# Kernel tuning notes

Measured on AMD Instinct MI355X. Metric: run time of the kernel, lower is better.

Reference implementation:

```python
import jax, jax.numpy as jnp
import numpy as np

B, N, D = 32, 4096, 256
HEADS, DH = 4, 64
DI = HEADS * DH  # 256
SLOTS, ITERS, EPS, HID = 8, 3, 1e-8, 128


def _ln(x, w, b):
    m = jnp.mean(x, axis=-1, keepdims=True)
    v = jnp.mean(jnp.square(x - m), axis=-1, keepdims=True)
    return (x - m) * jax.lax.rsqrt(v + 1e-5) * w + b


def setup_inputs() -> dict:
    key = jax.random.key(0)
    ks = jax.random.split(key, 12)
    g = lambda k, shape, s=0.05: jax.random.normal(k, shape, jnp.float32) * s
    return {
        "inputs": jax.random.normal(ks[0], (B, N, D), jnp.float32),
        "slots_mu": jax.random.normal(ks[1], (1, 1, D), jnp.float32),
        "slots_logsigma": g(ks[2], (1, 1, D), 0.1),
        "ln_in_w": jnp.ones((D,)), "ln_in_b": jnp.zeros((D,)),
        "ln_s_w": jnp.ones((D,)), "ln_s_b": jnp.zeros((D,)),
        "Wq": g(ks[3], (D, DI)), "Wk": g(ks[4], (D, DI)), "Wv": g(ks[5], (D, DI)),
        "Wc": g(ks[6], (DI, D)),
        "gru_w_ih": g(ks[7], (3 * D, D)), "gru_w_hh": g(ks[8], (3 * D, D)),
        "gru_b_ih": jnp.zeros((3 * D,)), "gru_b_hh": jnp.zeros((3 * D,)),
        "ln_m_w": jnp.ones((D,)), "ln_m_b": jnp.zeros((D,)),
        "mlp_w1": g(ks[9], (D, HID)), "mlp_b1": jnp.zeros((HID,)),
        "mlp_w2": g(ks[10], (HID, D)), "mlp_b2": jnp.zeros((D,)),
    }


def reference(inputs, slots_mu, slots_logsigma, ln_in_w, ln_in_b, ln_s_w, ln_s_b,
              Wq, Wk, Wv, Wc, gru_w_ih, gru_w_hh, gru_b_ih, gru_b_hh,
              ln_m_w, ln_m_b, mlp_w1, mlp_b1, mlp_w2, mlp_b2):
    b, n, d = inputs.shape
    scale = DH ** -0.5
    # slot initialization (fixed-seed gaussian, mirrors torch.manual_seed(0))
    noise = jax.random.normal(jax.random.key(42), (b, SLOTS, d), inputs.dtype)
    slots = slots_mu + jnp.exp(slots_logsigma) * noise

    x = _ln(inputs, ln_in_w, ln_in_b)
    k = (x @ Wk).reshape(b, n, HEADS, DH).transpose(0, 2, 1, 3)  # b h n dh
    v = (x @ Wv).reshape(b, n, HEADS, DH).transpose(0, 2, 1, 3)  # b h n dh

    for _ in range(ITERS):
        slots_prev = slots
        s = _ln(slots, ln_s_w, ln_s_b)
        q = (s @ Wq).reshape(b, SLOTS, HEADS, DH).transpose(0, 2, 1, 3)  # b h s dh
        dots = jnp.einsum('bhid,bhjd->bhij', q, k) * scale  # b h slots n
        attn = jax.nn.softmax(dots, axis=-2)  # softmax over SLOTS axis
        attn = attn + EPS
        attn = attn / jnp.sum(attn, axis=-1, keepdims=True)  # L1 norm over tokens
        updates = jnp.einsum('bhjd,bhij->bhid', v, attn)  # b h slots dh
        updates = updates.transpose(0, 2, 1, 3).reshape(b, SLOTS, DI) @ Wc  # b s d

        # GRUCell (PyTorch gate ordering: r, z, n)
        u = updates.reshape(-1, d)
        h = slots_prev.reshape(-1, d)
        gx = u @ gru_w_ih.T + gru_b_ih
        gh = h @ gru_w_hh.T + gru_b_hh
        xr, xz, xn = jnp.split(gx, 3, axis=-1)
        hr, hz, hn = jnp.split(gh, 3, axis=-1)
        r = jax.nn.sigmoid(xr + hr)
        z = jax.nn.sigmoid(xz + hz)
        ng = jnp.tanh(xn + r * hn)
        slots = ((1.0 - z) * ng + z * h).reshape(b, SLOTS, d)

        m = _ln(slots, ln_m_w, ln_m_b)
        slots = slots + (jax.nn.relu(m @ mlp_w1 + mlp_b1) @ mlp_w2 + mlp_b2)
    return slots
```

## Files before the change

kernel.cpp:

```cpp
#include <hip/hip_runtime.h>
#include <hip/hip_bf16.h>
#include <stdint.h>

constexpr int B_ = 32, N_ = 4096, D_ = 256, NH_ = 4, DH_ = 64, NS_ = 8;
constexpr float EPS_ = 1e-8f;

typedef unsigned short u16;
typedef __attribute__((ext_vector_type(8))) short bf16x8;
typedef __attribute__((ext_vector_type(4))) float f32x4;

__device__ inline u16 f2bf(float f) {
  unsigned u = __float_as_uint(f);
  unsigned r = u + 0x7FFFu + ((u >> 16) & 1u);
  return (u16)(r >> 16);
}
__device__ inline float bf2f(u16 u) {
  return __uint_as_float(((unsigned)u) << 16);
}

__device__ inline float erfinv_f(float x) {
  float w = -logf((1.0f - x) * (1.0f + x));
  float p;
  if (w < 5.0f) {
    w = w - 2.5f;
    p = 2.81022636e-08f;
    p = 3.43273939e-07f + p * w;
    p = -3.5233877e-06f + p * w;
    p = -4.39150654e-06f + p * w;
    p = 0.00021858087f + p * w;
    p = -0.00125372503f + p * w;
    p = -0.00417768164f + p * w;
    p = 0.246640727f + p * w;
    p = 1.50140941f + p * w;
  } else {
    w = sqrtf(w) - 3.0f;
    p = -0.000200214257f;
    p = 0.000100950558f + p * w;
    p = 0.00134934322f + p * w;
    p = -0.00367342844f + p * w;
    p = 0.00573950773f + p * w;
    p = -0.0076224613f + p * w;
    p = 0.00943887047f + p * w;
    p = 1.00167406f + p * w;
    p = 2.83297682f + p * w;
  }
  return p * x;
}

__device__ inline void threefry(unsigned k0, unsigned k1, unsigned& x0, unsigned& x1) {
  unsigned ks2 = k0 ^ k1 ^ 0x1BD11BDAu;
  x0 += k0; x1 += k1;
#define TF_R(r) { x0 += x1; x1 = (x1 << (r)) | (x1 >> (32 - (r))); x1 ^= x0; }
  TF_R(13) TF_R(15) TF_R(26) TF_R(6)
  x0 += k1; x1 += ks2 + 1u;
  TF_R(17) TF_R(29) TF_R(16) TF_R(24)
  x0 += ks2; x1 += k0 + 2u;
  TF_R(13) TF_R(15) TF_R(26) TF_R(6)
  x0 += k0; x1 += k1 + 3u;
  TF_R(17) TF_R(29) TF_R(16) TF_R(24)
  x0 += k1; x1 += ks2 + 4u;
  TF_R(13) TF_R(15) TF_R(26) TF_R(6)
  x0 += ks2; x1 += k0 + 5u;
#undef TF_R
}

__device__ inline float bits_to_normal(unsigned bits) {
  float f = __uint_as_float((bits >> 9) | 0x3F800000u) - 1.0f;
  const float lo = -0.99999994f;
  const float span = 2.0f;
  float u = fmaxf(lo, f * span + lo);
  return 1.41421356f * erfinv_f(u);
}

__global__ __launch_bounds__(256) void k_slots_init(const float* __restrict__ mu,
                                                    const float* __restrict__ logsigma,
                                                    float* __restrict__ slots) {
  unsigned e = blockIdx.x * 256u + threadIdx.x;
  unsigned x0 = 0u, x1 = e;
  threefry(0u, 42u, x0, x1);
  unsigned bits = x0 ^ x1;
  float n = bits_to_normal(bits);
  int d = e & 255;
  slots[e] = mu[d] + expf(logsigma[d]) * n;
}

__global__ __launch_bounds__(256) void k_qproj(const float* __restrict__ slots,
                                               const float* __restrict__ ln_w,
                                               const float* __restrict__ ln_b,
                                               const float* __restrict__ Wq,
                                               float* __restrict__ qout) {
  __shared__ float sn[256];
  __shared__ float redA[4], redB[4];
  int row = blockIdx.x, t = threadIdx.x;
  float x = slots[row * 256 + t];
  float s = x, s2 = x * x;
#pragma unroll
  for (int off = 32; off; off >>= 1) { s += __shfl_xor(s, off); s2 += __shfl_xor(s2, off); }
  if ((t & 63) == 0) { redA[t >> 6] = s; redB[t >> 6] = s2; }
  __syncthreads();
  float ts = redA[0] + redA[1] + redA[2] + redA[3];
  float ts2 = redB[0] + redB[1] + redB[2] + redB[3];
  float m = ts * (1.0f / 256.0f);
  float var = ts2 * (1.0f / 256.0f) - m * m;
  float rstd = rsqrtf(var + 1e-5f);
  sn[t] = (x - m) * rstd * ln_w[t] + ln_b[t];
  __syncthreads();
  float a = 0.0f;
  for (int k = 0; k < 256; ++k) a += sn[k] * Wq[k * 256 + t];
  qout[row * 256 + t] = a * 0.125f;
}

__global__ __launch_bounds__(256) void k_qproj2(const float* __restrict__ slots,
                                                const float* __restrict__ ln_w,
                                                const float* __restrict__ ln_b,
                                                const float* __restrict__ Wq,
                                                float* __restrict__ qout) {
  __shared__ float sn[256];
  __shared__ float part[4][64];
  __shared__ float redA[4], redB[4];
  int row = blockIdx.x, g = blockIdx.y, t = threadIdx.x;
  float x = slots[row * 256 + t];
  float s = x, s2 = x * x;
#pragma unroll
  for (int off = 32; off; off >>= 1) { s += __shfl_xor(s, off); s2 += __shfl_xor(s2, off); }
  if ((t & 63) == 0) { redA[t >> 6] = s; redB[t >> 6] = s2; }
  __syncthreads();
  float ts = redA[0] + redA[1] + redA[2] + redA[3];
  float ts2 = redB[0] + redB[1] + redB[2] + redB[3];
  float m = ts * (1.0f / 256.0f);
  float var = ts2 * (1.0f / 256.0f) - m * m;
  float rstd = rsqrtf(var + 1e-5f);
  sn[t] = (x - m) * rstd * ln_w[t] + ln_b[t];
  __syncthreads();
  int c = t & 63, kq = t >> 6;
  int col = g * 64 + c;
  float a = 0.0f;
#pragma unroll 8
  for (int k = kq * 64; k < kq * 64 + 64; ++k) a += sn[k] * Wq[k * 256 + col];
  part[kq][c] = a;
  __syncthreads();
  if (t < 64)
    qout[row * 256 + g * 64 + t] =
        (part[0][t] + part[1][t] + part[2][t] + part[3][t]) * 0.125f;
}

__global__ __launch_bounds__(256) void k_wt(const float* __restrict__ Wk,
                                            const float* __restrict__ Wv,
                                            u16* __restrict__ Wt) {
  int n = blockIdx.x;
  int t = threadIdx.x;
  const float* src = blockIdx.y ? Wv : Wk;
  Wt[((blockIdx.y * 256 + n) << 8) + t] = f2bf(src[t * 256 + n]);
}

__global__ __launch_bounds__(64) void k_wt2(const float* __restrict__ Wk,
                                            const float* __restrict__ Wv,
                                            u16* __restrict__ Wt2) {
  int cb = blockIdx.x, m = blockIdx.y, ks = blockIdx.z;
  int lane = threadIdx.x;
  const float* W = m ? Wv : Wk;
  int col = cb * 16 + (lane & 15);
  int kbase = ks * 32 + (lane >> 4) * 8;
  unsigned pk[4];
#pragma unroll
  for (int j = 0; j < 4; ++j) {
    u16 lo = f2bf(W[(long)(kbase + 2 * j) * 256 + col]);
    u16 hi = f2bf(W[(long)(kbase + 2 * j + 1) * 256 + col]);
    pk[j] = (unsigned)lo | ((unsigned)hi << 16);
  }
  *(uint4*)&Wt2[(long)(((m * 16 + cb) * 8 + ks) * 64 + lane) * 8] =
      make_uint4(pk[0], pk[1], pk[2], pk[3]);
}

__global__ __launch_bounds__(256) void k_gru_t(const float* __restrict__ src,
                                               float* __restrict__ dst) {
  __shared__ float tile[32][33];
  int c0 = blockIdx.x * 32;
  int r0 = blockIdx.y * 32;
  int tx = threadIdx.x & 31, ty = threadIdx.x >> 5;
#pragma unroll
  for (int i = 0; i < 32; i += 8)
    tile[ty + i][tx] = src[(long)(r0 + ty + i) * 256 + c0 + tx];
  __syncthreads();
#pragma unroll
  for (int i = 0; i < 32; i += 8)
    dst[(long)(c0 + ty + i) * 768 + r0 + tx] = tile[tx][ty + i];
}

__global__ __launch_bounds__(512, 4) void k_proj_mfma3(
    const float* __restrict__ in,
    const float* __restrict__ ln_w, const float* __restrict__ ln_b,
    const u16* __restrict__ Wt2,
    u16* __restrict__ kbuf, u16* __restrict__ vbuf) {
  constexpr int LDA = 264;
  __shared__ __align__(16) u16 lds[18432];
  u16* Asm = lds;
  int t = threadIdx.x;
  int w = t >> 6, lane = t & 63;
  int q = lane >> 4, r = lane & 15;
  long row0 = (long)blockIdx.x * 64;
  int m = w >> 2;

  float4 lw = ((const float4*)ln_w)[lane];
  float4 lb = ((const float4*)ln_b)[lane];
  float4 vr[8];
#pragma unroll
  for (int j = 0; j < 8; ++j)
    vr[j] = ((const float4*)(in + (row0 + w * 8 + j) * D_))[lane];
#pragma unroll
  for (int j = 0; j < 8; ++j) {
    int rr = w * 8 + j;
    float4 v = vr[j];
    float s = v.x + v.y + v.z + v.w;
    float s2 = v.x * v.x + v.y * v.y + v.z * v.z + v.w * v.w;
#pragma unroll
    for (int off = 32; off; off >>= 1) { s += __shfl_xor(s, off); s2 += __shfl_xor(s2, off); }
    float mn = s * (1.0f / 256.0f);
    float var = s2 * (1.0f / 256.0f) - mn * mn;
    float rstd = rsqrtf(var + 1e-5f);
    unsigned p0 = (unsigned)f2bf((v.x - mn) * rstd * lw.x + lb.x)
                | ((unsigned)f2bf((v.y - mn) * rstd * lw.y + lb.y) << 16);
    unsigned p1 = (unsigned)f2bf((v.z - mn) * rstd * lw.z + lb.z)
                | ((unsigned)f2bf((v.w - mn) * rstd * lw.w + lb.w) << 16);
    *(uint2*)&Asm[rr * LDA + lane * 4] = make_uint2(p0, p1);
  }
  __syncthreads();

  f32x4 acc[4][4];
#pragma unroll
  for (int mf = 0; mf < 4; ++mf)
#pragma unroll
    for (int nf = 0; nf < 4; ++nf) acc[mf][nf] = (f32x4)0.0f;

#pragma unroll 2
  for (int ks = 0; ks < 8; ++ks) {
    int k0 = ks * 32;
    bf16x8 a[4], b[4];
#pragma unroll
    for (int mf = 0; mf < 4; ++mf)
      a[mf] = *(const bf16x8*)&Asm[(mf * 16 + r) * LDA + k0 + q * 8];
#pragma unroll
    for (int nf = 0; nf < 4; ++nf)
      b[nf] = *(const bf16x8*)&Wt2[(long)(((m * 16 + (w & 3) * 4 + nf) * 8 + ks) * 64 + lane) * 8];
#pragma unroll
    for (int mf = 0; mf < 4; ++mf)
#pragma unroll
      for (int nf = 0; nf < 4; ++nf)
        acc[mf][nf] = __builtin_amdgcn_mfma_f32_16x16x32_bf16(a[mf], b[nf], acc[mf][nf], 0, 0, 0);
  }

  __syncthreads();
  u16* st = lds + w * 2304;
  u16* outp = m ? vbuf : kbuf;
  int colbase = (w & 3) * 64;
#pragma unroll
  for (int p = 0; p < 2; ++p) {
#pragma unroll
    for (int mfh = 0; mfh < 2; ++mfh) {
      int mf = p * 2 + mfh;
#pragma unroll
      for (int nf = 0; nf < 4; ++nf)
#pragma unroll
        for (int rr = 0; rr < 4; ++rr) {
          int rowp = mfh * 16 + q * 4 + rr;
          int col = nf * 16 + r;
          int colsw = col ^ ((rowp & 7) << 3);
          st[rowp * 72 + colsw] = f2bf(acc[mf][nf][rr]);
        }
    }
#pragma unroll
    for (int sub = 0; sub < 4; ++sub) {
      int rowp = sub * 8 + (lane >> 3);
      int c8 = (lane & 7) * 8;
      int c8s = c8 ^ ((rowp & 7) << 3);
      uint4 val = *(const uint4*)&st[rowp * 72 + c8s];
      *(uint4*)&outp[(row0 + p * 32 + rowp) * 256 + colbase + c8] = val;
    }
  }
}

__global__ __launch_bounds__(512, 4) void k_proj_mfma2(
    const float* __restrict__ in,
    const float* __restrict__ ln_w, const float* __restrict__ ln_b,
    const u16* __restrict__ Wt,
    u16* __restrict__ kbuf, u16* __restrict__ vbuf) {
  constexpr int LDA = 264;
  __shared__ __align__(16) u16 Asm[64 * LDA];
  int t = threadIdx.x;
  int w = t >> 6, lane = t & 63;
  int q = lane >> 4, r = lane & 15;
  long row0 = (long)blockIdx.x * 64;
  int half = blockIdx.y;

  float4 lw = ((const float4*)ln_w)[lane];
  float4 lb = ((const float4*)ln_b)[lane];
#pragma unroll 4
  for (int j = 0; j < 8; ++j) {
    int rr = w * 8 + j;
    float4 v = ((const float4*)(in + (row0 + rr) * D_))[lane];
    float s = v.x + v.y + v.z + v.w;
    float s2 = v.x * v.x + v.y * v.y + v.z * v.z + v.w * v.w;
#pragma unroll
    for (int off = 32; off; off >>= 1) { s += __shfl_xor(s, off); s2 += __shfl_xor(s2, off); }
    float m = s * (1.0f / 256.0f);
    float var = s2 * (1.0f / 256.0f) - m * m;
    float rstd = rsqrtf(var + 1e-5f);
    unsigned p0 = (unsigned)f2bf((v.x - m) * rstd * lw.x + lb.x)
                | ((unsigned)f2bf((v.y - m) * rstd * lw.y + lb.y) << 16);
    unsigned p1 = (unsigned)f2bf((v.z - m) * rstd * lw.z + lb.z)
                | ((unsigned)f2bf((v.w - m) * rstd * lw.w + lb.w) << 16);
    *(uint2*)&Asm[rr * LDA + lane * 4] = make_uint2(p0, p1);
  }
  __syncthreads();

  f32x4 acc[4][2];
#pragma unroll
  for (int mf = 0; mf < 4; ++mf)
#pragma unroll
    for (int nf = 0; nf < 2; ++nf) acc[mf][nf] = (f32x4)0.0f;

  const u16* wt_base = Wt + (long)(half * 256 + w * 32) * 256;
#pragma unroll 2
  for (int k0 = 0; k0 < 256; k0 += 32) {
    bf16x8 a[4], b[2];
#pragma unroll
    for (int mf = 0; mf < 4; ++mf)
      a[mf] = *(const bf16x8*)&Asm[(mf * 16 + r) * LDA + k0 + q * 8];
#pragma unroll
    for (int nf = 0; nf < 2; ++nf)
      b[nf] = *(const bf16x8*)&wt_base[(nf * 16 + r) * 256 + k0 + q * 8];
#pragma unroll
    for (int mf = 0; mf < 4; ++mf)
#pragma unroll
      for (int nf = 0; nf < 2; ++nf)
        acc[mf][nf] = __builtin_amdgcn_mfma_f32_16x16x32_bf16(a[mf], b[nf], acc[mf][nf], 0, 0, 0);
  }

  __syncthreads();
  u16* st = Asm + w * 1280;
  u16* outp = half ? vbuf : kbuf;
#pragma unroll
  for (int p = 0; p < 2; ++p) {
#pragma unroll
    for (int m2 = 0; m2 < 2; ++m2)
#pragma unroll
      for (int nf = 0; nf < 2; ++nf)
#pragma unroll
        for (int rr = 0; rr < 4; ++rr)
          st[(m2 * 16 + q * 4 + rr) * 40 + nf * 16 + r] = f2bf(acc[p * 2 + m2][nf][rr]);
#pragma unroll
    for (int s = 0; s < 2; ++s) {
      int rw = s * 16 + (lane >> 2);
      int cc = (lane & 3) * 8;
      uint4 val = *(const uint4*)&st[rw * 40 + cc];
      *(uint4*)&outp[(row0 + p * 32 + rw) * 256 + w * 32 + cc] = val;
    }
  }
}

__global__ __launch_bounds__(256) void k_attn(
    const float* __restrict__ qbuf,
    const u16* __restrict__ kbuf, const u16* __restrict__ vbuf,
    float* __restrict__ U, float* __restrict__ S) {
  __shared__ float redS[2048];
  __shared__ float sredS[32];
  int b = blockIdx.y, chunk = blockIdx.x;
  int t = threadIdx.x;
  int wave = t >> 6, lane = t & 63;

  for (int e = t; e < 2048; e += 256) redS[e] = 0.0f;
  if (t < 32) sredS[t] = 0.0f;

  float qv[8][4];
#pragma unroll
  for (int i = 0; i < 8; ++i) {
    float4 qq = *(const float4*)(qbuf + ((long)(b * 8 + i)) * 256 + lane * 4);
    qv[i][0] = qq.x; qv[i][1] = qq.y; qv[i][2] = qq.z; qv[i][3] = qq.w;
  }
  float acc[8][4];
  float sacc[8];
#pragma unroll
  for (int i = 0; i < 8; ++i) {
    sacc[i] = 0.0f;
    acc[i][0] = acc[i][1] = acc[i][2] = acc[i][3] = 0.0f;
  }
  __syncthreads();

  long jbase = (long)b * N_ + chunk * 128;
  for (int jj = wave; jj < 128; jj += 4) {
    long off = (jbase + jj) * 256 + lane * 4;
    ushort4 k4 = *(const ushort4*)(kbuf + off);
    ushort4 v4 = *(const ushort4*)(vbuf + off);
    float k0 = bf2f(k4.x), k1 = bf2f(k4.y), k2 = bf2f(k4.z), k3 = bf2f(k4.w);

    float d[8];
#pragma unroll
    for (int i = 0; i < 8; ++i)
      d[i] = qv[i][0] * k0 + qv[i][1] * k1 + qv[i][2] * k2 + qv[i][3] * k3;
#pragma unroll
    for (int off2 = 1; off2 < 16; off2 <<= 1) {
#pragma unroll
      for (int i = 0; i < 8; ++i) d[i] += __shfl_xor(d[i], off2);
    }
    float mx = d[0];
#pragma unroll
    for (int i = 1; i < 8; ++i) mx = fmaxf(mx, d[i]);
    float e[8], sum = 0.0f;
#pragma unroll
    for (int i = 0; i < 8; ++i) { e[i] = expf(d[i] - mx); sum += e[i]; }
    float inv = 1.0f / sum;

    float v0 = bf2f(v4.x), v1 = bf2f(v4.y), v2 = bf2f(v4.z), v3 = bf2f(v4.w);
#pragma unroll
    for (int i = 0; i < 8; ++i) {
      float a = e[i] * inv + EPS_;
      sacc[i] += a;
      acc[i][0] += a * v0; acc[i][1] += a * v1; acc[i][2] += a * v2; acc[i][3] += a * v3;
    }
  }

#pragma unroll
  for (int i = 0; i < 8; ++i) {
    atomicAdd(&redS[i * 256 + lane * 4 + 0], acc[i][0]);
    atomicAdd(&redS[i * 256 + lane * 4 + 1], acc[i][1]);
    atomicAdd(&redS[i * 256 + lane * 4 + 2], acc[i][2]);
    atomicAdd(&redS[i * 256 + lane * 4 + 3], acc[i][3]);
  }
  if ((lane & 15) == 0) {
    int h = lane >> 4;
#pragma unroll
    for (int i = 0; i < 8; ++i) atomicAdd(&sredS[i * 4 + h], sacc[i]);
  }
  __syncthreads();

  for (int e = t; e < 2048; e += 256)
    atomicAdd(&U[((long)b * 8 + (e >> 8)) * 256 + (e & 255)], redS[e]);
  if (t < 32) atomicAdd(&S[b * 32 + t], sredS[t]);
}

__global__ __launch_bounds__(256) void k_attn3(
    const float* __restrict__ qbuf,
    const u16* __restrict__ kbuf, const u16* __restrict__ vbuf,
    float* __restrict__ P, float* __restrict__ Sp) {
  __shared__ __align__(16) u16 Ks[64 * 260];
  __shared__ __align__(16) float qs[8 * 256];
  __shared__ float dw[64 * 33];
  int b = blockIdx.y, chunk = blockIdx.x;
  int t = threadIdx.x;
  int tok = t & 63;
  int sp = t >> 6;

  for (int e = t; e < 2048; e += 256) qs[e] = qbuf[(long)b * 2048 + e];

  float acc0[4] = {0.f, 0.f, 0.f, 0.f};
  float acc1[4] = {0.f, 0.f, 0.f, 0.f};
  float rden[8] = {0.f, 0.f, 0.f, 0.f, 0.f, 0.f, 0.f, 0.f};

  long tokbase = (long)b * N_ + chunk * 128;
  for (int tile = 0; tile < 2; ++tile) {
    long trow = tokbase + tile * 64;
    __syncthreads();
#pragma unroll
    for (int i = 0; i < 16; ++i) {
      int idx = i * 256 + t;
      int row = idx >> 6, c8 = idx & 63;
      *(uint2*)&Ks[row * 260 + c8 * 4] =
          *(const uint2*)&kbuf[(trow + row) * 256 + c8 * 4];
    }
    __syncthreads();

    float d0[4] = {0.f, 0.f, 0.f, 0.f};
    float d1[4] = {0.f, 0.f, 0.f, 0.f};
#pragma unroll
    for (int h = 0; h < 4; ++h) {
#pragma unroll
      for (int c2 = 0; c2 < 8; ++c2) {
        int cc = h * 8 + c2;
        ushort4 ka = *(const ushort4*)&Ks[tok * 260 + cc * 8];
        ushort4 kb = *(const ushort4*)&Ks[tok * 260 + cc * 8 + 4];
        float k0 = bf2f(ka.x), k1 = bf2f(ka.y), k2 = bf2f(ka.z), k3 = bf2f(ka.w);
        float k4 = bf2f(kb.x), k5 = bf2f(kb.y), k6 = bf2f(kb.z), k7 = bf2f(kb.w);
        float4 qa0 = *(const float4*)&qs[(sp * 2) * 256 + cc * 8];
        float4 qa1 = *(const float4*)&qs[(sp * 2) * 256 + cc * 8 + 4];
        float4 qb0 = *(const float4*)&qs[(sp * 2 + 1) * 256 + cc * 8];
        float4 qb1 = *(const float4*)&qs[(sp * 2 + 1) * 256 + cc * 8 + 4];
        d0[h] += qa0.x * k0 + qa0.y * k1 + qa0.z * k2 + qa0.w * k3
               + qa1.x * k4 + qa1.y * k5 + qa1.z * k6 + qa1.w * k7;
        d1[h] += qb0.x * k0 + qb0.y * k1 + qb0.z * k2 + qb0.w * k3
               + qb1.x * k4 + qb1.y * k5 + qb1.z * k6 + qb1.w * k7;
      }
    }
#pragma unroll
    for (int h = 0; h < 4; ++h) {
      dw[tok * 33 + (sp * 2) * 4 + h] = d0[h];
      dw[tok * 33 + (sp * 2 + 1) * 4 + h] = d1[h];
    }
    __syncthreads();

    {
      float dv[8];
#pragma unroll
      for (int i = 0; i < 8; ++i) dv[i] = dw[tok * 33 + i * 4 + sp];
      float mx = dv[0];
#pragma unroll
      for (int i = 1; i < 8; ++i) mx = fmaxf(mx, dv[i]);
      float sum = 0.f;
#pragma unroll
      for (int i = 0; i < 8; ++i) { dv[i] = expf(dv[i] - mx); sum += dv[i]; }
      float inv = 1.0f / sum;
#pragma unroll
      for (int i = 0; i < 8; ++i) {
        float a = dv[i] * inv + EPS_;
        dw[tok * 33 + i * 4 + sp] = a;
        rden[i] += a;
      }
    }
    __syncthreads();

    {
      int col = tok * 4;
      int h = tok >> 4;
      int wbase0 = (sp * 2) * 4 + h;
      int wbase1 = (sp * 2 + 1) * 4 + h;
#pragma unroll 4
      for (int j = 0; j < 64; ++j) {
        float w0 = dw[j * 33 + wbase0];
        float w1 = dw[j * 33 + wbase1];
        ushort4 vv = *(const ushort4*)&vbuf[(trow + j) * 256 + col];
        float v0 = bf2f(vv.x), v1 = bf2f(vv.y), v2 = bf2f(vv.z), v3 = bf2f(vv.w);
        acc0[0] += w0 * v0; acc0[1] += w0 * v1; acc0[2] += w0 * v2; acc0[3] += w0 * v3;
        acc1[0] += w1 * v0; acc1[1] += w1 * v1; acc1[2] += w1 * v2; acc1[3] += w1 * v3;
      }
    }
  }

  long pbase = ((long)chunk * 32 + b) * 2048;
  {
    int col = tok * 4;
    *(float4*)&P[pbase + (sp * 2) * 256 + col] = make_float4(acc0[0], acc0[1], acc0[2], acc0[3]);
    *(float4*)&P[pbase + (sp * 2 + 1) * 256 + col] = make_float4(acc1[0], acc1[1], acc1[2], acc1[3]);
  }
#pragma unroll
  for (int i = 0; i < 8; ++i) {
#pragma unroll
    for (int off = 32; off; off >>= 1) rden[i] += __shfl_xor(rden[i], off);
  }
  if (tok == 0) {
#pragma unroll
    for (int i = 0; i < 8; ++i)
      Sp[((long)chunk * 32 + b) * 32 + i * 4 + sp] = rden[i];
  }
}

__global__ __launch_bounds__(256) void k_slot_update(
    const float* __restrict__ U, const float* __restrict__ S,
    float* __restrict__ slots,
    const float* __restrict__ Wc,
    const float* __restrict__ w_ih, const float* __restrict__ w_hh,
    const float* __restrict__ b_ih, const float* __restrict__ b_hh,
    const float* __restrict__ ln_m_w, const float* __restrict__ ln_m_b,
    const float* __restrict__ w1, const float* __restrict__ b1,
    const float* __restrict__ w2, const float* __restrict__ b2,
    float* __restrict__ out_final, int write_out) {
  __shared__ float un[256], upd[256], hprev[256], mbuf[256], hid[128];
  __shared__ float redA[4], redB[4];
  int row = blockIdx.x, t = threadIdx.x;

  float denom = S[row * 4 + (t >> 6)];
  un[t] = U[(long)row * 256 + t] / denom;
  float hp = slots[(long)row * 256 + t];
  hprev[t] = hp;
  __syncthreads();

  float a = 0.0f;
  for (int k = 0; k < 256; ++k) a += un[k] * Wc[k * 256 + t];
  upd[t] = a;
  __syncthreads();

  float gxr = b_ih[t], gxz = b_ih[256 + t], gxn = b_ih[512 + t];
  float ghr = b_hh[t], ghz = b_hh[256 + t], ghn = b_hh[512 + t];
  const float4* u4 = (const float4*)upd;
  const float4* h4 = (const float4*)hprev;
  const float4* wr = (const float4*)(w_ih + (long)t * 256);
  const float4* wz = (const float4*)(w_ih + (long)(256 + t) * 256);
  const float4* wn = (const float4*)(w_ih + (long)(512 + t) * 256);
  const float4* vr = (const float4*)(w_hh + (long)t * 256);
  const float4* vz = (const float4*)(w_hh + (long)(256 + t) * 256);
  const float4* vn = (const float4*)(w_hh + (long)(512 + t) * 256);
  for (int k = 0; k < 64; ++k) {
    float4 uu = u4[k], hh = h4[k], w;
    w = wr[k]; gxr += uu.x * w.x + uu.y * w.y + uu.z * w.z + uu.w * w.w;
    w = wz[k]; gxz += uu.x * w.x + uu.y * w.y + uu.z * w.z + uu.w * w.w;
    w = wn[k]; gxn += uu.x * w.x + uu.y * w.y + uu.z * w.z + uu.w * w.w;
    w = vr[k]; ghr += hh.x * w.x + hh.y * w.y + hh.z * w.z + hh.w * w.w;
    w = vz[k]; ghz += hh.x * w.x + hh.y * w.y + hh.z * w.z + hh.w * w.w;
    w = vn[k]; ghn += hh.x * w.x + hh.y * w.y + hh.z * w.z + hh.w * w.w;
  }
  float r = 1.0f / (1.0f + expf(-(gxr + ghr)));
  float z = 1.0f / (1.0f + expf(-(gxz + ghz)));
  float ng = tanhf(gxn + r * ghn);
  float sv = (1.0f - z) * ng + z * hp;

  float s1 = sv, s2v = sv * sv;
#pragma unroll
  for (int off = 32; off; off >>= 1) { s1 += __shfl_xor(s1, off); s2v += __shfl_xor(s2v, off); }
  if ((t & 63) == 0) { redA[t >> 6] = s1; redB[t >> 6] = s2v; }
  __syncthreads();
  float ts = redA[0] + redA[1] + redA[2] + redA[3];
  float ts2 = redB[0] + redB[1] + redB[2] + redB[3];
  float mean = ts * (1.0f / 256.0f);
  float var = ts2 * (1.0f / 256.0f) - mean * mean;
  float rstd = rsqrtf(var + 1e-5f);
  mbuf[t] = (sv - mean) * rstd * ln_m_w[t] + ln_m_b[t];
  __syncthreads();

  if (t < 128) {
    float hv = b1[t];
    for (int d = 0; d < 256; ++d) hv += mbuf[d] * w1[d * 128 + t];
    hid[t] = fmaxf(hv, 0.0f);
  }
  __syncthreads();
  float o = b2[t];
  for (int j = 0; j < 128; ++j) o += hid[j] * w2[j * 256 + t];
  float res = sv + o;
  slots[(long)row * 256 + t] = res;
  if (write_out) out_final[(long)row * 256 + t] = res;
}

__global__ __launch_bounds__(768) void k_slot_update3(
    const float* __restrict__ P, const float* __restrict__ Sp,
    float* __restrict__ slots,
    const float* __restrict__ Wc,
    const float* __restrict__ wTih, const float* __restrict__ wThh,
    const float* __restrict__ b_ih, const float* __restrict__ b_hh,
    const float* __restrict__ ln_m_w, const float* __restrict__ ln_m_b,
    const float* __restrict__ w1, const float* __restrict__ b1,
    const float* __restrict__ w2, const float* __restrict__ b2,
    float* __restrict__ out_final, int write_out) {
  __shared__ float un[256], upd[256], hprev[256], mbuf[256], hid[128];
  __shared__ float updS[3][256];
  __shared__ float gxs[768], ghs[768];
  __shared__ float redA[4], redB[4];
  int row = blockIdx.x, t = threadIdx.x;

  if (t < 256) {
    int b = row >> 3, sl = row & 7, h = t >> 6;
    float au = 0.0f, dn = 0.0f;
#pragma unroll 4
    for (int c = 0; c < 32; ++c) {
      au += P[(((long)c * 32 + b) * 8 + sl) * 256 + t];
      dn += Sp[((long)c * 32 + b) * 32 + sl * 4 + h];
    }
    un[t] = au / dn;
    hprev[t] = slots[(long)row * 256 + t];
  }
  __syncthreads();

  {
    int c = t & 255, s = t >> 8;
    int k0 = s * 85, k1 = (s == 2) ? 256 : (k0 + 85);
    float a = 0.0f;
    for (int k = k0; k < k1; ++k) a += un[k] * Wc[k * 256 + c];
    updS[s][c] = a;
  }
  __syncthreads();
  if (t < 256) upd[t] = updS[0][t] + updS[1][t] + updS[2][t];
  __syncthreads();

  {
    float gx = b_ih[t], gh = b_hh[t];
#pragma unroll 4
    for (int k = 0; k < 256; ++k) {
      float uk = upd[k], hk = hprev[k];
      gx += uk * wTih[(long)k * 768 + t];
      gh += hk * wThh[(long)k * 768 + t];
    }
    gxs[t] = gx; ghs[t] = gh;
  }
  __syncthreads();

  float sv = 0.0f;
  if (t < 256) {
    float r = 1.0f / (1.0f + expf(-(gxs[t] + ghs[t])));
    float z = 1.0f / (1.0f + expf(-(gxs[256 + t] + ghs[256 + t])));
    float ng = tanhf(gxs[512 + t] + r * ghs[512 + t]);
    sv = (1.0f - z) * ng + z * hprev[t];
    float s1 = sv, s2v = sv * sv;
#pragma unroll
    for (int off = 32; off; off >>= 1) { s1 += __shfl_xor(s1, off); s2v += __shfl_xor(s2v, off); }
    if ((t & 63) == 0) { redA[t >> 6] = s1; redB[t >> 6] = s2v; }
  }
  __syncthreads();
  if (t < 256) {
    float ts = redA[0] + redA[1] + redA[2] + redA[3];
    float ts2 = redB[0] + redB[1] + redB[2] + redB[3];
    float mean = ts * (1.0f / 256.0f);
    float var = ts2 * (1.0f / 256.0f) - mean * mean;
    float rstd = rsqrtf(var + 1e-5f);
    mbuf[t] = (sv - mean) * rstd * ln_m_w[t] + ln_m_b[t];
  }
  __syncthreads();
  if (t < 128) {
    float hv = b1[t];
    for (int d = 0; d < 256; ++d) hv += mbuf[d] * w1[d * 128 + t];
    hid[t] = fmaxf(hv, 0.0f);
  }
  __syncthreads();
  if (t < 256) {
    float o = b2[t];
    for (int j = 0; j < 128; ++j) o += hid[j] * w2[j * 256 + t];
    float res = sv + o;
    slots[(long)row * 256 + t] = res;
    if (write_out) out_final[(long)row * 256 + t] = res;
  }
}

__global__ __launch_bounds__(256) void k_fused_attn(
    const float* __restrict__ in,
    const float* __restrict__ ln_w, const float* __restrict__ ln_b,
    const float* __restrict__ Wk, const float* __restrict__ Wv,
    const float* __restrict__ qbuf,
    float* __restrict__ U, float* __restrict__ S) {
  __shared__ __align__(16) float ldsf[24576];
  float* xs = ldsf;
  float* kf = ldsf + 8192;
  float* vf = ldsf + 16384;
  float* qs    = ldsf;
  float* redS  = ldsf + 2048;
  float* sredS = ldsf + 4096;

  int b = blockIdx.y, chunk = blockIdx.x;
  int t = threadIdx.x;
  int wave = t >> 6, lane = t & 63;
  long row0 = (long)b * N_ + (long)chunk * 32;

  for (int j = 0; j < 8; ++j) {
    int r = wave * 8 + j;
    const float4* rp = (const float4*)(in + (row0 + r) * D_);
    float4 v = rp[lane];
    float s = v.x + v.y + v.z + v.w;
    float s2 = v.x * v.x + v.y * v.y + v.z * v.z + v.w * v.w;
#pragma unroll
    for (int off = 32; off; off >>= 1) { s += __shfl_xor(s, off); s2 += __shfl_xor(s2, off); }
    float m = s * (1.0f / 256.0f);
    float var = s2 * (1.0f / 256.0f) - m * m;
    float rstd = rsqrtf(var + 1e-5f);
    int c = lane * 4;
    xs[r * 256 + c + 0] = (v.x - m) * rstd * ln_w[c + 0] + ln_b[c + 0];
    xs[r * 256 + c + 1] = (v.y - m) * rstd * ln_w[c + 1] + ln_b[c + 1];
    xs[r * 256 + c + 2] = (v.z - m) * rstd * ln_w[c + 2] + ln_b[c + 2];
    xs[r * 256 + c + 3] = (v.w - m) * rstd * ln_w[c + 3] + ln_b[c + 3];
  }
  __syncthreads();

  {
    int tx = t & 31, ty = t >> 5;
    const float* W = (tx < 16) ? Wk : Wv;
    float* obf = (tx < 16) ? kf : vf;
    int col0 = (tx & 15) * 16;
    float acc2[4][16];
#pragma unroll
    for (int r = 0; r < 4; ++r)
#pragma unroll
      for (int c = 0; c < 16; ++c) acc2[r][c] = 0.0f;

    for (int k = 0; k < 256; ++k) {
      const float4* wp = (const float4*)(W + k * 256 + col0);
      float4 w0 = wp[0], w1 = wp[1], w2 = wp[2], w3 = wp[3];
#pragma unroll
      for (int r = 0; r < 4; ++r) {
        float x = xs[(ty * 4 + r) * 256 + k];
        acc2[r][0]  += x * w0.x; acc2[r][1]  += x * w0.y; acc2[r][2]  += x * w0.z; acc2[r][3]  += x * w0.w;
        acc2[r][4]  += x * w1.x; acc2[r][5]  += x * w1.y; acc2[r][6]  += x * w1.z; acc2[r][7]  += x * w1.w;
        acc2[r][8]  += x * w2.x; acc2[r][9]  += x * w2.y; acc2[r][10] += x * w2.z; acc2[r][11] += x * w2.w;
        acc2[r][12] += x * w3.x; acc2[r][13] += x * w3.y; acc2[r][14] += x * w3.z; acc2[r][15] += x * w3.w;
      }
    }
#pragma unroll
    for (int r = 0; r < 4; ++r) {
      float4* dst = (float4*)&obf[(ty * 4 + r) * 256 + col0];
      dst[0] = make_float4(acc2[r][0],  acc2[r][1],  acc2[r][2],  acc2[r][3]);
      dst[1] = make_float4(acc2[r][4],  acc2[r][5],  acc2[r][6],  acc2[r][7]);
      dst[2] = make_float4(acc2[r][8],  acc2[r][9],  acc2[r][10], acc2[r][11]);
      dst[3] = make_float4(acc2[r][12], acc2[r][13], acc2[r][14], acc2[r][15]);
    }
  }
  __syncthreads();

#pragma unroll
  for (int i = 0; i < 8; ++i) qs[i * 256 + t] = qbuf[((long)b * 8 + i) * 256 + t];
  for (int e = t; e < 2048; e += 256) redS[e] = 0.0f;
  if (t < 32) sredS[t] = 0.0f;
  __syncthreads();

  float qv[8][4];
#pragma unroll
  for (int i = 0; i < 8; ++i) {
    float4 qq = *(const float4*)&qs[i * 256 + lane * 4];
    qv[i][0] = qq.x; qv[i][1] = qq.y; qv[i][2] = qq.z; qv[i][3] = qq.w;
  }
  float acc[8][4];
  float sacc[8];
#pragma unroll
  for (int i = 0; i < 8; ++i) {
    sacc[i] = 0.0f;
    acc[i][0] = acc[i][1] = acc[i][2] = acc[i][3] = 0.0f;
  }

  for (int jj = wave; jj < 32; jj += 4) {
    float4 k4 = *(const float4*)&kf[jj * 256 + lane * 4];
    float d[8];
#pragma unroll
    for (int i = 0; i < 8; ++i)
      d[i] = qv[i][0] * k4.x + qv[i][1] * k4.y + qv[i][2] * k4.z + qv[i][3] * k4.w;
#pragma unroll
    for (int off2 = 1; off2 < 16; off2 <<= 1) {
#pragma unroll
      for (int i = 0; i < 8; ++i) d[i] += __shfl_xor(d[i], off2);
    }
    float mx = d[0];
#pragma unroll
    for (int i = 1; i < 8; ++i) mx = fmaxf(mx, d[i]);
    float e[8], sum = 0.0f;
#pragma unroll
    for (int i = 0; i < 8; ++i) { e[i] = expf(d[i] - mx); sum += e[i]; }
    float inv = 1.0f / sum;

    float4 v4 = *(const float4*)&vf[jj * 256 + lane * 4];
#pragma unroll
    for (int i = 0; i < 8; ++i) {
      float a = e[i] * inv + EPS_;
      sacc[i] += a;
      acc[i][0] += a * v4.x; acc[i][1] += a * v4.y; acc[i][2] += a * v4.z; acc[i][3] += a * v4.w;
    }
  }

#pragma unroll
  for (int i = 0; i < 8; ++i) {
    atomicAdd(&redS[i * 256 + lane * 4 + 0], acc[i][0]);
    atomicAdd(&redS[i * 256 + lane * 4 + 1], acc[i][1]);
    atomicAdd(&redS[i * 256 + lane * 4 + 2], acc[i][2]);
    atomicAdd(&redS[i * 256 + lane * 4 + 3], acc[i][3]);
  }
  if ((lane & 15) == 0) {
    int h = lane >> 4;
#pragma unroll
    for (int i = 0; i < 8; ++i) atomicAdd(&sredS[i * 4 + h], sacc[i]);
  }
  __syncthreads();

  for (int e = t; e < 2048; e += 256)
    atomicAdd(&U[((long)b * 8 + (e >> 8)) * 256 + (e & 255)], redS[e]);
  if (t < 32) atomicAdd(&S[b * 32 + t], sredS[t]);
}

extern "C" void kernel_launch(void* const* d_in, const int* in_sizes, int n_in,
                              void* d_out, int out_size, void* d_ws, size_t ws_size,
                              hipStream_t stream) {
  (void)in_sizes; (void)n_in; (void)out_size;
  const float* inputs        = (const float*)d_in[0];
  const float* slots_mu      = (const float*)d_in[1];
  const float* slots_logsig  = (const float*)d_in[2];
  const float* ln_in_w       = (const float*)d_in[3];
  const float* ln_in_b       = (const float*)d_in[4];
  const float* ln_s_w        = (const float*)d_in[5];
  const float* ln_s_b        = (const float*)d_in[6];
  const float* Wq            = (const float*)d_in[7];
  const float* Wk            = (const float*)d_in[8];
  const float* Wv            = (const float*)d_in[9];
  const float* Wc            = (const float*)d_in[10];
  const float* w_ih          = (const float*)d_in[11];
  const float* w_hh          = (const float*)d_in[12];
  const float* b_ih          = (const float*)d_in[13];
  const float* b_hh          = (const float*)d_in[14];
  const float* ln_m_w        = (const float*)d_in[15];
  const float* ln_m_b        = (const float*)d_in[16];
  const float* w1            = (const float*)d_in[17];
  const float* b1            = (const float*)d_in[18];
  const float* w2            = (const float*)d_in[19];
  const float* b2            = (const float*)d_in[20];

  const size_t KV_BYTES = 2ull * 32 * 4096 * 256 * sizeof(u16);
  char* ws = (char*)d_ws;

  if (ws_size >= KV_BYTES + (12ull << 20)) {
    u16* kbuf    = (u16*)ws;
    u16* vbuf    = (u16*)(ws + KV_BYTES / 2);
    char* base   = ws + KV_BYTES;
    float* slots = (float*)base;
    float* qbuf  = (float*)(base + (256ull << 10));
    u16*   Wt2   = (u16*)(base + (256ull << 10));
    float* P     = (float*)(base + (512ull << 10));
    float* Sp    = (float*)(base + (512ull << 10) + (8ull << 20));
    float* wTih  = (float*)(base + (512ull << 10) + (8ull << 20) + (128ull << 10));
    float* wThh  = (float*)(base + (512ull << 10) + (8ull << 20) + (128ull << 10) + (768ull << 10));

    k_slots_init<<<256, 256, 0, stream>>>(slots_mu, slots_logsig, slots);
    k_gru_t<<<dim3(8, 24), 256, 0, stream>>>(w_ih, wTih);
    k_gru_t<<<dim3(8, 24), 256, 0, stream>>>(w_hh, wThh);
    k_wt2<<<dim3(16, 2, 8), 64, 0, stream>>>(Wk, Wv, Wt2);
    k_proj_mfma3<<<2048, 512, 0, stream>>>(inputs, ln_in_w, ln_in_b, Wt2, kbuf, vbuf);

    for (int it = 0; it < 3; ++it) {
      k_qproj2<<<dim3(256, 4), 256, 0, stream>>>(slots, ln_s_w, ln_s_b, Wq, qbuf);
      k_attn3<<<dim3(32, 32), 256, 0, stream>>>(qbuf, kbuf, vbuf, P, Sp);
      k_slot_update3<<<256, 768, 0, stream>>>(P, Sp, slots, Wc, wTih, wThh, b_ih, b_hh,
                                              ln_m_w, ln_m_b, w1, b1, w2, b2,
                                              (float*)d_out, it == 2 ? 1 : 0);
    }
  } else if (ws_size >= KV_BYTES + (1ull << 20)) {
    u16* kbuf    = (u16*)ws;
    u16* vbuf    = (u16*)(ws + KV_BYTES / 2);
    char* base   = ws + KV_BYTES;
    float* slots = (float*)base;
    float* qbuf  = (float*)(base + 262144);
    float* U     = (float*)(base + 524288);
    float* S     = (float*)(base + 786432);
    u16* Wt      = (u16*)(base + 262144);

    k_slots_init<<<256, 256, 0, stream>>>(slots_mu, slots_logsig, slots);
    k_wt<<<dim3(256, 2), 256, 0, stream>>>(Wk, Wv, Wt);
    k_proj_mfma2<<<dim3(2048, 2), 512, 0, stream>>>(inputs, ln_in_w, ln_in_b, Wt, kbuf, vbuf);

    for (int it = 0; it < 3; ++it) {
      hipMemsetAsync(U, 0, (65536 + 1024) * sizeof(float), stream);
      k_qproj<<<256, 256, 0, stream>>>(slots, ln_s_w, ln_s_b, Wq, qbuf);
      k_attn<<<dim3(32, 32), 256, 0, stream>>>(qbuf, kbuf, vbuf, U, S);
      k_slot_update<<<256, 256, 0, stream>>>(U, S, slots, Wc, w_ih, w_hh, b_ih, b_hh,
                                             ln_m_w, ln_m_b, w1, b1, w2, b2,
                                             (float*)d_out, it == 2 ? 1 : 0);
    }
  } else {
    float* slots = (float*)ws;
    float* qbuf  = (float*)(ws + 262144);
    float* U     = (float*)(ws + 524288);
    float* S     = (float*)(ws + 786432);

    k_slots_init<<<256, 256, 0, stream>>>(slots_mu, slots_logsig, slots);
    for (int it = 0; it < 3; ++it) {
      hipMemsetAsync(U, 0, (65536 + 1024) * sizeof(float), stream);
      k_qproj<<<256, 256, 0, stream>>>(slots, ln_s_w, ln_s_b, Wq, qbuf);
      k_fused_attn<<<dim3(128, 32), 256, 0, stream>>>(inputs, ln_in_w, ln_in_b,
                                                      Wk, Wv, qbuf, U, S);
      k_slot_update<<<256, 256, 0, stream>>>(U, S, slots, Wc, w_ih, w_hh, b_ih, b_hh,
                                             ln_m_w, ln_m_b, w1, b1, w2, b2,
                                             (float*)d_out, it == 2 ? 1 : 0);
    }
  }
}
```

Baseline: 656.4 us.

## Use MFMA for slot attention and store V transposed per head

Rewrites the attention kernel to compute q·k dots and the attn·V product with bf16 MFMA instructions, using one wavefront per head. Softmax over slots is done in registers with cross-lane shuffles instead of round-trips through shared memory. The projection kernel now writes V in a per-batch transposed (feature × token) layout so V rows feed MFMA B-operands directly, and its LDS A-tile uses an XOR swizzle instead of padding. The cost is that q and attention weights are rounded to bf16, and half of each 16-row MFMA tile is wasted because there are only 8 slots.

```diff
diff --git a/kernel.cpp b/kernel.cpp
--- a/kernel.cpp
+++ b/kernel.cpp
@@ -187,14 +187,12 @@
     dst[(long)(c0 + ty + i) * 768 + r0 + tx] = tile[tx][ty + i];
 }
 
-__global__ __launch_bounds__(512, 4) void k_proj_mfma3(
+__global__ __launch_bounds__(512, 4) void k_proj_mfma4(
     const float* __restrict__ in,
     const float* __restrict__ ln_w, const float* __restrict__ ln_b,
     const u16* __restrict__ Wt2,
-    u16* __restrict__ kbuf, u16* __restrict__ vbuf) {
-  constexpr int LDA = 264;
-  __shared__ __align__(16) u16 lds[18432];
-  u16* Asm = lds;
+    u16* __restrict__ kbuf, u16* __restrict__ vt) {
+  __shared__ __align__(16) u16 lds[16384];
   int t = threadIdx.x;
   int w = t >> 6, lane = t & 63;
   int q = lane >> 4, r = lane & 15;
@@ -222,7 +220,8 @@
                 | ((unsigned)f2bf((v.y - mn) * rstd * lw.y + lb.y) << 16);
     unsigned p1 = (unsigned)f2bf((v.z - mn) * rstd * lw.z + lb.z)
                 | ((unsigned)f2bf((v.w - mn) * rstd * lw.w + lb.w) << 16);
-    *(uint2*)&Asm[rr * LDA + lane * 4] = make_uint2(p0, p1);
+    int unit = (lane >> 1) ^ (rr & 7);
+    *(uint2*)&lds[rr * 256 + unit * 8 + (lane & 1) * 4] = make_uint2(p0, p1);
   }
   __syncthreads();
 
@@ -234,11 +233,12 @@
 
 #pragma unroll 2
   for (int ks = 0; ks < 8; ++ks) {
-    int k0 = ks * 32;
     bf16x8 a[4], b[4];
 #pragma unroll
-    for (int mf = 0; mf < 4; ++mf)
-      a[mf] = *(const bf16x8*)&Asm[(mf * 16 + r) * LDA + k0 + q * 8];
+    for (int mf = 0; mf < 4; ++mf) {
+      int unit = ((ks * 4 + q) ^ (r & 7));
+      a[mf] = *(const bf16x8*)&lds[(mf * 16 + r) * 256 + unit * 8];
+    }
 #pragma unroll
     for (int nf = 0; nf < 4; ++nf)
       b[nf] = *(const bf16x8*)&Wt2[(long)(((m * 16 + (w & 3) * 4 + nf) * 8 + ks) * 64 + lane) * 8];
@@ -250,32 +250,46 @@
   }
 
   __syncthreads();
-  u16* st = lds + w * 2304;
-  u16* outp = m ? vbuf : kbuf;
-  int colbase = (w & 3) * 64;
-#pragma unroll
-  for (int p = 0; p < 2; ++p) {
-#pragma unroll
-    for (int mfh = 0; mfh < 2; ++mfh) {
-      int mf = p * 2 + mfh;
-#pragma unroll
-      for (int nf = 0; nf < 4; ++nf)
-#pragma unroll
-        for (int rr = 0; rr < 4; ++rr) {
-          int rowp = mfh * 16 + q * 4 + rr;
-          int col = nf * 16 + r;
-          int colsw = col ^ ((rowp & 7) << 3);
-          st[rowp * 72 + colsw] = f2bf(acc[mf][nf][rr]);
-        }
-    }
-#pragma unroll
-    for (int sub = 0; sub < 4; ++sub) {
-      int rowp = sub * 8 + (lane >> 3);
-      int c8 = (lane & 7) * 8;
-      int c8s = c8 ^ ((rowp & 7) << 3);
-      uint4 val = *(const uint4*)&st[rowp * 72 + c8s];
-      *(uint4*)&outp[(row0 + p * 32 + rowp) * 256 + colbase + c8] = val;
-    }
+  if (m == 0) {
+    u16* st = lds + w * 2304;
+    int colbase = (w & 3) * 64;
+#pragma unroll
+    for (int p = 0; p < 2; ++p) {
+#pragma unroll
+      for (int mfh = 0; mfh < 2; ++mfh) {
+        int mf = p * 2 + mfh;
+#pragma unroll
+        for (int nf = 0; nf < 4; ++nf)
+#pragma unroll
+          for (int rr = 0; rr < 4; ++rr) {
+            int rowp = mfh * 16 + q * 4 + rr;
+            int col = nf * 16 + r;
+            int colsw = col ^ ((rowp & 7) << 3);
+            st[rowp * 72 + colsw] = f2bf(acc[mf][nf][rr]);
+          }
+      }
+#pragma unroll
+      for (int sub = 0; sub < 4; ++sub) {
+        int rowp = sub * 8 + (lane >> 3);
+        int c8 = (lane & 7) * 8;
+        int c8s = c8 ^ ((rowp & 7) << 3);
+        uint4 val = *(const uint4*)&st[rowp * 72 + c8s];
+        *(uint4*)&kbuf[(row0 + p * 32 + rowp) * 256 + colbase + c8] = val;
+      }
+    }
+  } else {
+    int bb = (int)(row0 >> 12);
+    int tloc = (int)(row0 & 4095);
+    int colb = (w & 3) * 64;
+#pragma unroll
+    for (int mf = 0; mf < 4; ++mf)
+#pragma unroll
+      for (int nf = 0; nf < 4; ++nf) {
+        unsigned p0 = (unsigned)f2bf(acc[mf][nf][0]) | ((unsigned)f2bf(acc[mf][nf][1]) << 16);
+        unsigned p1 = (unsigned)f2bf(acc[mf][nf][2]) | ((unsigned)f2bf(acc[mf][nf][3]) << 16);
+        long dst = ((long)bb * 256 + colb + nf * 16 + r) * 4096 + tloc + mf * 16 + q * 4;
+        *(uint2*)&vt[dst] = make_uint2(p0, p1);
+      }
   }
 }
 
@@ -438,117 +452,103 @@
   if (t < 32) atomicAdd(&S[b * 32 + t], sredS[t]);
 }
 
-__global__ __launch_bounds__(256) void k_attn3(
+__global__ __launch_bounds__(256) void k_attn4(
     const float* __restrict__ qbuf,
-    const u16* __restrict__ kbuf, const u16* __restrict__ vbuf,
+    const u16* __restrict__ kbuf, const u16* __restrict__ vt,
     float* __restrict__ P, float* __restrict__ Sp) {
-  __shared__ __align__(16) u16 Ks[64 * 260];
-  __shared__ __align__(16) float qs[8 * 256];
-  __shared__ float dw[64 * 33];
+  __shared__ __align__(16) u16 abuf[4][16 * 128];
   int b = blockIdx.y, chunk = blockIdx.x;
   int t = threadIdx.x;
-  int tok = t & 63;
-  int sp = t >> 6;
-
-  for (int e = t; e < 2048; e += 256) qs[e] = qbuf[(long)b * 2048 + e];
-
-  float acc0[4] = {0.f, 0.f, 0.f, 0.f};
-  float acc1[4] = {0.f, 0.f, 0.f, 0.f};
-  float rden[8] = {0.f, 0.f, 0.f, 0.f, 0.f, 0.f, 0.f, 0.f};
-
-  long tokbase = (long)b * N_ + chunk * 128;
-  for (int tile = 0; tile < 2; ++tile) {
-    long trow = tokbase + tile * 64;
-    __syncthreads();
-#pragma unroll
-    for (int i = 0; i < 16; ++i) {
-      int idx = i * 256 + t;
-      int row = idx >> 6, c8 = idx & 63;
-      *(uint2*)&Ks[row * 260 + c8 * 4] =
-          *(const uint2*)&kbuf[(trow + row) * 256 + c8 * 4];
-    }
-    __syncthreads();
-
-    float d0[4] = {0.f, 0.f, 0.f, 0.f};
-    float d1[4] = {0.f, 0.f, 0.f, 0.f};
-#pragma unroll
-    for (int h = 0; h < 4; ++h) {
-#pragma unroll
-      for (int c2 = 0; c2 < 8; ++c2) {
-        int cc = h * 8 + c2;
-        ushort4 ka = *(const ushort4*)&Ks[tok * 260 + cc * 8];
-        ushort4 kb = *(const ushort4*)&Ks[tok * 260 + cc * 8 + 4];
-        float k0 = bf2f(ka.x), k1 = bf2f(ka.y), k2 = bf2f(ka.z), k3 = bf2f(ka.w);
-        float k4 = bf2f(kb.x), k5 = bf2f(kb.y), k6 = bf2f(kb.z), k7 = bf2f(kb.w);
-        float4 qa0 = *(const float4*)&qs[(sp * 2) * 256 + cc * 8];
-        float4 qa1 = *(const float4*)&qs[(sp * 2) * 256 + cc * 8 + 4];
-        float4 qb0 = *(const float4*)&qs[(sp * 2 + 1) * 256 + cc * 8];
-        float4 qb1 = *(const float4*)&qs[(sp * 2 + 1) * 256 + cc * 8 + 4];
-        d0[h] += qa0.x * k0 + qa0.y * k1 + qa0.z * k2 + qa0.w * k3
-               + qa1.x * k4 + qa1.y * k5 + qa1.z * k6 + qa1.w * k7;
-        d1[h] += qb0.x * k0 + qb0.y * k1 + qb0.z * k2 + qb0.w * k3
-               + qb1.x * k4 + qb1.y * k5 + qb1.z * k6 + qb1.w * k7;
+  int h = t >> 6, lane = t & 63;
+  int q = lane >> 4, r = lane & 15;
+  long tok0 = (long)b * N_ + chunk * 128;
+
+  bf16x8 aq[2];
+  {
+    union { u16 us[8]; bf16x8 v; } pk;
+#pragma unroll
+    for (int i = 0; i < 8; ++i) pk.us[i] = 0;
+    aq[0] = pk.v; aq[1] = pk.v;
+    if (r < 8) {
+#pragma unroll
+      for (int c = 0; c < 2; ++c) {
+        const float* qp = qbuf + (long)b * 2048 + r * 256 + h * 64 + c * 32 + q * 8;
+        float4 qa = *(const float4*)qp;
+        float4 qb = *(const float4*)(qp + 4);
+        pk.us[0] = f2bf(qa.x); pk.us[1] = f2bf(qa.y);
+        pk.us[2] = f2bf(qa.z); pk.us[3] = f2bf(qa.w);
+        pk.us[4] = f2bf(qb.x); pk.us[5] = f2bf(qb.y);
+        pk.us[6] = f2bf(qb.z); pk.us[7] = f2bf(qb.w);
+        aq[c] = pk.v;
       }
     }
-#pragma unroll
-    for (int h = 0; h < 4; ++h) {
-      dw[tok * 33 + (sp * 2) * 4 + h] = d0[h];
-      dw[tok * 33 + (sp * 2 + 1) * 4 + h] = d1[h];
-    }
-    __syncthreads();
-
-    {
-      float dv[8];
-#pragma unroll
-      for (int i = 0; i < 8; ++i) dv[i] = dw[tok * 33 + i * 4 + sp];
-      float mx = dv[0];
-#pragma unroll
-      for (int i = 1; i < 8; ++i) mx = fmaxf(mx, dv[i]);
-      float sum = 0.f;
-#pragma unroll
-      for (int i = 0; i < 8; ++i) { dv[i] = expf(dv[i] - mx); sum += dv[i]; }
-      float inv = 1.0f / sum;
-#pragma unroll
-      for (int i = 0; i < 8; ++i) {
-        float a = dv[i] * inv + EPS_;
-        dw[tok * 33 + i * 4 + sp] = a;
-        rden[i] += a;
+  }
+
+  u16* ab = abuf[h];
+  float rden[4] = {0.f, 0.f, 0.f, 0.f};
+
+#pragma unroll 2
+  for (int tg = 0; tg < 8; ++tg) {
+    long krow = tok0 + tg * 16 + r;
+    bf16x8 bk0 = *(const bf16x8*)&kbuf[krow * 256 + h * 64 + q * 8];
+    bf16x8 bk1 = *(const bf16x8*)&kbuf[krow * 256 + h * 64 + 32 + q * 8];
+    f32x4 d = (f32x4)0.0f;
+    d = __builtin_amdgcn_mfma_f32_16x16x32_bf16(aq[0], bk0, d, 0, 0, 0);
+    d = __builtin_amdgcn_mfma_f32_16x16x32_bf16(aq[1], bk1, d, 0, 0, 0);
+    float mx = fmaxf(fmaxf(d[0], d[1]), fmaxf(d[2], d[3]));
+    mx = fmaxf(mx, __shfl_xor(mx, 16));
+    float e0 = expf(d[0] - mx), e1 = expf(d[1] - mx);
+    float e2 = expf(d[2] - mx), e3 = expf(d[3] - mx);
+    float sum = e0 + e1 + e2 + e3;
+    sum += __shfl_xor(sum, 16);
+    float inv = 1.0f / sum;
+    float av[4] = {e0 * inv + EPS_, e1 * inv + EPS_, e2 * inv + EPS_, e3 * inv + EPS_};
+    int col = tg * 16 + r;
+#pragma unroll
+    for (int i = 0; i < 4; ++i) {
+      u16 ab16 = 0;
+      if (q < 2) {
+        ab16 = f2bf(av[i]);
+        rden[i] += bf2f(ab16);
       }
-    }
-    __syncthreads();
-
-    {
-      int col = tok * 4;
-      int h = tok >> 4;
-      int wbase0 = (sp * 2) * 4 + h;
-      int wbase1 = (sp * 2 + 1) * 4 + h;
-#pragma unroll 4
-      for (int j = 0; j < 64; ++j) {
-        float w0 = dw[j * 33 + wbase0];
-        float w1 = dw[j * 33 + wbase1];
-        ushort4 vv = *(const ushort4*)&vbuf[(trow + j) * 256 + col];
-        float v0 = bf2f(vv.x), v1 = bf2f(vv.y), v2 = bf2f(vv.z), v3 = bf2f(vv.w);
-        acc0[0] += w0 * v0; acc0[1] += w0 * v1; acc0[2] += w0 * v2; acc0[3] += w0 * v3;
-        acc1[0] += w1 * v0; acc1[1] += w1 * v1; acc1[2] += w1 * v2; acc1[3] += w1 * v3;
-      }
+      int rowi = q * 4 + i;
+      int unit = (col >> 3) ^ (rowi & 7);
+      ab[rowi * 128 + unit * 8 + (col & 7)] = ab16;
+    }
+  }
+
+#pragma unroll
+  for (int i = 0; i < 4; ++i) {
+#pragma unroll
+    for (int off = 1; off < 16; off <<= 1) rden[i] += __shfl_xor(rden[i], off);
+  }
+
+  f32x4 au[4];
+#pragma unroll
+  for (int nf = 0; nf < 4; ++nf) au[nf] = (f32x4)0.0f;
+#pragma unroll
+  for (int ks = 0; ks < 4; ++ks) {
+    bf16x8 pa = *(const bf16x8*)&ab[r * 128 + (((ks * 4 + q) ^ (r & 7)) * 8)];
+#pragma unroll
+    for (int nf = 0; nf < 4; ++nf) {
+      bf16x8 bv = *(const bf16x8*)&vt[((long)b * 256 + h * 64 + nf * 16 + r) * 4096
+                                      + chunk * 128 + ks * 32 + q * 8];
+      au[nf] = __builtin_amdgcn_mfma_f32_16x16x32_bf16(pa, bv, au[nf], 0, 0, 0);
     }
   }
 
   long pbase = ((long)chunk * 32 + b) * 2048;
-  {
-    int col = tok * 4;
-    *(float4*)&P[pbase + (sp * 2) * 256 + col] = make_float4(acc0[0], acc0[1], acc0[2], acc0[3]);
-    *(float4*)&P[pbase + (sp * 2 + 1) * 256 + col] = make_float4(acc1[0], acc1[1], acc1[2], acc1[3]);
-  }
-#pragma unroll
-  for (int i = 0; i < 8; ++i) {
-#pragma unroll
-    for (int off = 32; off; off >>= 1) rden[i] += __shfl_xor(rden[i], off);
-  }
-  if (tok == 0) {
-#pragma unroll
-    for (int i = 0; i < 8; ++i)
-      Sp[((long)chunk * 32 + b) * 32 + i * 4 + sp] = rden[i];
+  if (q < 2) {
+#pragma unroll
+    for (int nf = 0; nf < 4; ++nf)
+#pragma unroll
+      for (int i = 0; i < 4; ++i)
+        P[pbase + (q * 4 + i) * 256 + h * 64 + nf * 16 + r] = au[nf][i];
+    if (r == 0) {
+#pragma unroll
+      for (int i = 0; i < 4; ++i)
+        Sp[((long)chunk * 32 + b) * 32 + (q * 4 + i) * 4 + h] = rden[i];
+    }
   }
 }
 
@@ -584,17 +584,17 @@
   const float4* wr = (const float4*)(w_ih + (long)t * 256);
   const float4* wz = (const float4*)(w_ih + (long)(256 + t) * 256);
   const float4* wn = (const float4*)(w_ih + (long)(512 + t) * 256);
-  const float4* vr = (const float4*)(w_hh + (long)t * 256);
-  const float4* vz = (const float4*)(w_hh + (long)(256 + t) * 256);
-  const float4* vn = (const float4*)(w_hh + (long)(512 + t) * 256);
+  const float4* vrp = (const float4*)(w_hh + (long)t * 256);
+  const float4* vzp = (const float4*)(w_hh + (long)(256 + t) * 256);
+  const float4* vnp = (const float4*)(w_hh + (long)(512 + t) * 256);
   for (int k = 0; k < 64; ++k) {
     float4 uu = u4[k], hh = h4[k], w;
-    w = wr[k]; gxr += uu.x * w.x + uu.y * w.y + uu.z * w.z + uu.w * w.w;
-    w = wz[k]; gxz += uu.x * w.x + uu.y * w.y + uu.z * w.z + uu.w * w.w;
-    w = wn[k]; gxn += uu.x * w.x + uu.y * w.y + uu.z * w.z + uu.w * w.w;
-    w = vr[k]; ghr += hh.x * w.x + hh.y * w.y + hh.z * w.z + hh.w * w.w;
-    w = vz[k]; ghz += hh.x * w.x + hh.y * w.y + hh.z * w.z + hh.w * w.w;
-    w = vn[k]; ghn += hh.x * w.x + hh.y * w.y + hh.z * w.z + hh.w * w.w;
+    w = wr[k];  gxr += uu.x * w.x + uu.y * w.y + uu.z * w.z + uu.w * w.w;
+    w = wz[k];  gxz += uu.x * w.x + uu.y * w.y + uu.z * w.z + uu.w * w.w;
+    w = wn[k];  gxn += uu.x * w.x + uu.y * w.y + uu.z * w.z + uu.w * w.w;
+    w = vrp[k]; ghr += hh.x * w.x + hh.y * w.y + hh.z * w.z + hh.w * w.w;
+    w = vzp[k]; ghz += hh.x * w.x + hh.y * w.y + hh.z * w.z + hh.w * w.w;
+    w = vnp[k]; ghn += hh.x * w.x + hh.y * w.y + hh.z * w.z + hh.w * w.w;
   }
   float r = 1.0f / (1.0f + expf(-(gxr + ghr)));
   float z = 1.0f / (1.0f + expf(-(gxz + ghz)));
@@ -885,7 +885,7 @@
 
   if (ws_size >= KV_BYTES + (12ull << 20)) {
     u16* kbuf    = (u16*)ws;
-    u16* vbuf    = (u16*)(ws + KV_BYTES / 2);
+    u16* Vt      = (u16*)(ws + KV_BYTES / 2);
     char* base   = ws + KV_BYTES;
     float* slots = (float*)base;
     float* qbuf  = (float*)(base + (256ull << 10));
@@ -899,11 +899,11 @@
     k_gru_t<<<dim3(8, 24), 256, 0, stream>>>(w_ih, wTih);
     k_gru_t<<<dim3(8, 24), 256, 0, stream>>>(w_hh, wThh);
     k_wt2<<<dim3(16, 2, 8), 64, 0, stream>>>(Wk, Wv, Wt2);
-    k_proj_mfma3<<<2048, 512, 0, stream>>>(inputs, ln_in_w, ln_in_b, Wt2, kbuf, vbuf);
+    k_proj_mfma4<<<2048, 512, 0, stream>>>(inputs, ln_in_w, ln_in_b, Wt2, kbuf, Vt);
 
     for (int it = 0; it < 3; ++it) {
       k_qproj2<<<dim3(256, 4), 256, 0, stream>>>(slots, ln_s_w, ln_s_b, Wq, qbuf);
-      k_attn3<<<dim3(32, 32), 256, 0, stream>>>(qbuf, kbuf, vbuf, P, Sp);
+      k_attn4<<<dim3(32, 32), 256, 0, stream>>>(qbuf, kbuf, Vt, P, Sp);
       k_slot_update3<<<256, 768, 0, stream>>>(P, Sp, slots, Wc, wTih, wThh, b_ih, b_hh,
                                               ln_m_w, ln_m_b, w1, b1, w2, b2,
                                               (float*)d_out, it == 2 ? 1 : 0);
```

Result: faster. 564.8 us (-14.0%).
